# Kernel tuning notes

Hardware: AMD Instinct MI355X
Metric: run time of the kernel (lower is better)

The kernel has to match this reference:

```python
import jax, jax.numpy as jnp
import numpy as np

B, H, E, V, T, EOS = 128, 512, 256, 32000, 32, 0

def setup_inputs() -> dict:
    key = jax.random.key(0)
    ks = jax.random.split(key, 10)
    s_emb = 1.0 / np.sqrt(V)
    s_rnn = 1.0 / np.sqrt(H)
    return {
        "z": jax.random.normal(ks[0], (B, H), jnp.float32),
        "W_emb": jax.random.uniform(ks[1], (E, V), jnp.float32, -s_emb, s_emb),
        "b_emb": jax.random.uniform(ks[2], (E,), jnp.float32, -s_emb, s_emb),
        "W_ih": jax.random.uniform(ks[3], (H, E), jnp.float32, -s_rnn, s_rnn),
        "b_ih": jax.random.uniform(ks[4], (H,), jnp.float32, -s_rnn, s_rnn),
        "W_hh": jax.random.uniform(ks[5], (H, H), jnp.float32, -s_rnn, s_rnn),
        "b_hh": jax.random.uniform(ks[6], (H,), jnp.float32, -s_rnn, s_rnn),
        "W_lin": jax.random.uniform(ks[7], (V, H), jnp.float32, -s_rnn, s_rnn),
        "b_lin": jax.random.uniform(ks[8], (V,), jnp.float32, -s_rnn, s_rnn),
        "train": 0,
    }

def _emit(hidden, W_lin, b_lin):
    # [B,H] @ [H,V] -> log_p [B,V]; greedy (argmax) decode path (train=False)
    log_p = jax.nn.log_softmax(hidden @ W_lin.T + b_lin, axis=-1)
    sample = jnp.argmax(log_p, axis=-1)                       # [B] int
    symb = jax.nn.one_hot(sample, V, dtype=log_p.dtype)       # [B,V]
    lp_tok = jnp.take_along_axis(log_p, sample[:, None], axis=1)[:, 0]
    return symb, lp_tok

def reference(z, W_emb, b_emb, W_ih, b_ih, W_hh, b_hh, W_lin, b_lin, train):
    # step 0: hidden = z, no RNN update
    symb, lp_tok = _emit(z, W_lin, b_lin)
    log_p_sent = lp_tok
    mask = 1.0 - symb[:, EOS]

    def step(carry, _):
        hidden, symb, log_p_sent, mask = carry
        emb = symb @ W_emb.T + b_emb                          # one-hot "embedding" linear
        hidden = jnp.tanh(emb @ W_ih.T + b_ih + hidden @ W_hh.T + b_hh)  # Elman RNN cell
        symb, lp_tok = _emit(hidden, W_lin, b_lin)
        log_p_sent = log_p_sent + mask * lp_tok
        mask = mask * (1.0 - symb[:, EOS])
        return (hidden, symb, log_p_sent, mask), symb

    (_, _, log_p_sent, _), rest = jax.lax.scan(step, (z, symb, log_p_sent, mask), None, length=T - 1)
    sentences = jnp.concatenate([symb[None], rest], axis=0)   # [T,B,V]
    return sentences, log_p_sent
```

## Files before the change

### kernel.cpp

```cpp
#include <hip/hip_runtime.h>
#include <math.h>

constexpr int NB = 128;
constexpr int NH = 512;
constexpr int NE = 256;
constexpr int NV = 32000;
constexpr int NT = 32;
constexpr int NVBW = 1000;

typedef _Float16 half8 __attribute__((ext_vector_type(8)));
typedef float    f32x4 __attribute__((ext_vector_type(4)));

#define AGLD(p)    __hip_atomic_load((p), __ATOMIC_RELAXED, __HIP_MEMORY_SCOPE_AGENT)
#define AGST(p, v) __hip_atomic_store((p), (v), __ATOMIC_RELAXED, __HIP_MEMORY_SCOPE_AGENT)

__global__ void init_kernel(unsigned* cnt) { *cnt = 0u; }

__device__ __forceinline__ void gsync(unsigned* cnt, unsigned target) {
    asm volatile("s_waitcnt vmcnt(0) lgkmcnt(0)" ::: "memory");
    __syncthreads();
    if (threadIdx.x == 0) {
        __hip_atomic_fetch_add(cnt, 1u, __ATOMIC_RELAXED, __HIP_MEMORY_SCOPE_AGENT);
        while (AGLD(cnt) < target) __builtin_amdgcn_s_sleep(4);
    }
    __syncthreads();
    asm volatile("" ::: "memory");
}

__global__ __launch_bounds__(512, 2)
void speaker_kernel(const float* __restrict__ z,    const float* __restrict__ Wemb,
                    const float* __restrict__ bemb, const float* __restrict__ Wih,
                    const float* __restrict__ bih,  const float* __restrict__ Whh,
                    const float* __restrict__ bhh,  const float* __restrict__ Wlin,
                    const float* __restrict__ blin, float* __restrict__ out,
                    _Float16* __restrict__ Wh,      unsigned long long* __restrict__ hidh64,
                    float* __restrict__ hid,
                    float* __restrict__ pm1, int* __restrict__ pi1,
                    float* __restrict__ pm2, int* __restrict__ pi2,
                    float* __restrict__ ps,  float* __restrict__ lps,
                    float* __restrict__ maskp, unsigned* __restrict__ cnt)
{
    __shared__ _Float16 smA[128][64];
    __shared__ _Float16 smB[2][128][64];
    __shared__ float red8[8];
    __shared__ int   cand[32];
    __shared__ float cval[32];
    __shared__ int   ncand;
    __shared__ int   besti;
    __shared__ float es[NE];
    __shared__ float hs[NH];
    __shared__ _Float16 hsout[NH];

    const int blk  = blockIdx.x;
    const int tid  = threadIdx.x;
    const int w    = tid >> 6;
    const int lane = tid & 63;
    const int gtid = blk * 512 + tid;
    constexpr int GT = 256 * 512;
    unsigned sno = 0;

    unsigned long long* Wh64 = (unsigned long long*)Wh;

    for (int i = gtid; i < NV * NH / 4; i += GT) {
        float4 a = ((const float4*)Wlin)[i];
        union { _Float16 h[4]; unsigned long long u; } p;
        p.h[0] = (_Float16)a.x; p.h[1] = (_Float16)a.y;
        p.h[2] = (_Float16)a.z; p.h[3] = (_Float16)a.w;
        AGST(Wh64 + i, p.u);
    }
    for (int i = gtid; i < NB * NH / 4; i += GT) {
        float4 a = ((const float4*)z)[i];
        union { _Float16 h[4]; unsigned long long u; } p;
        p.h[0] = (_Float16)a.x; p.h[1] = (_Float16)a.y;
        p.h[2] = (_Float16)a.z; p.h[3] = (_Float16)a.w;
        AGST(hidh64 + i, p.u);
    }
    ++sno; gsync(cnt, sno * 256u);

    for (int t = 0; t < NT; t++) {
        if (blk < 250) {
            const int wm = w >> 2;
            const int wn = w & 3;
            const int v0 = blk * 128;

            const _Float16* gpB[2];
            unsigned ldsoffB[2];
#pragma unroll
            for (int c = 0; c < 2; c++) {
                int slot = w * 128 + c * 64 + lane;
                int r    = slot >> 3;
                int sp   = slot & 7;
                int g    = sp ^ (r & 7);
                gpB[c] = Wh + (size_t)(v0 + r) * NH + g * 8;
                ldsoffB[c] = (unsigned)(w * 128 + c * 64) * 16;
            }
#define STAGE_B(dbuf, k0)                                                      \
    do {                                                                       \
        _Pragma("unroll")                                                      \
        for (int c = 0; c < 2; c++) {                                          \
            __builtin_amdgcn_global_load_lds(                                  \
                (const __attribute__((address_space(1))) unsigned*)(gpB[c] + (k0)), \
                (__attribute__((address_space(3))) unsigned*)((char*)&smB[0][0][0] + (dbuf)*16384 + ldsoffB[c]), \
                16, 0, 0);                                                     \
        }                                                                      \
    } while (0)

            const int ar   = tid >> 2;
            const int asp0 = (tid & 3) * 2;
            const int ag0  = asp0 ^ (ar & 7);
            const int ag1  = (asp0 + 1) ^ (ar & 7);
            const unsigned long long* hbase = hidh64 + ar * 128;

            f32x4 acc[4][2];
#pragma unroll
            for (int mi = 0; mi < 4; mi++)
#pragma unroll
                for (int ni = 0; ni < 2; ni++) acc[mi][ni] = {0.f, 0.f, 0.f, 0.f};

            unsigned long long a0, a1, a2, a3;
            a0 = AGLD(hbase + ag0 * 2);     a1 = AGLD(hbase + ag0 * 2 + 1);
            a2 = AGLD(hbase + ag1 * 2);     a3 = AGLD(hbase + ag1 * 2 + 1);
            STAGE_B(0, 0);

#pragma unroll
            for (int kt = 0; kt < 8; kt++) {
                {
                    unsigned long long* dA = (unsigned long long*)&smA[ar][asp0 * 8];
                    dA[0] = a0; dA[1] = a1; dA[2] = a2; dA[3] = a3;
                }
                if (kt < 7) {
                    const unsigned long long* hb = hbase + (kt + 1) * 16;
                    a0 = AGLD(hb + ag0 * 2); a1 = AGLD(hb + ag0 * 2 + 1);
                    a2 = AGLD(hb + ag1 * 2); a3 = AGLD(hb + ag1 * 2 + 1);
                    STAGE_B((kt + 1) & 1, (kt + 1) * 64);
                }
                __builtin_amdgcn_sched_barrier(0);
                if (kt < 7) asm volatile("s_waitcnt vmcnt(6)" ::: "memory");
                else        asm volatile("s_waitcnt vmcnt(0)" ::: "memory");
                __builtin_amdgcn_sched_barrier(0);
                __syncthreads();

#pragma unroll
                for (int kk = 0; kk < 2; kk++) {
                    const int sbase = kk * 4 + (lane >> 4);
                    half8 af[4], bf[2];
#pragma unroll
                    for (int mi = 0; mi < 4; mi++) {
                        int r = wm * 64 + mi * 16 + (lane & 15);
                        af[mi] = *(const half8*)&smA[r][(sbase ^ (r & 7)) * 8];
                    }
#pragma unroll
                    for (int ni = 0; ni < 2; ni++) {
                        int rb = wn * 32 + ni * 16 + (lane & 15);
                        bf[ni] = *(const half8*)&smB[kt & 1][rb][(sbase ^ (rb & 7)) * 8];
                    }
#pragma unroll
                    for (int mi = 0; mi < 4; mi++)
#pragma unroll
                        for (int ni = 0; ni < 2; ni++)
                            acc[mi][ni] = __builtin_amdgcn_mfma_f32_16x16x32_f16(
                                af[mi], bf[ni], acc[mi][ni], 0, 0, 0);
                }
                __syncthreads();
            }
#undef STAGE_B

            const int colbase = v0 + wn * 32 + (lane & 15);
            const float bias0 = blin[colbase];
            const float bias1 = blin[colbase + 16];
            const int cidx = blk * 4 + wn;

#pragma unroll
            for (int mi = 0; mi < 4; mi++) {
#pragma unroll
                for (int reg = 0; reg < 4; reg++) {
                    const int bRow = wm * 64 + mi * 16 + (lane >> 4) * 4 + reg;
                    const float va = acc[mi][0][reg] + bias0;
                    const float vc = acc[mi][1][reg] + bias1;
                    float v1, v2; int j1, j2;
                    if (va >= vc) { v1 = va; j1 = colbase;      v2 = vc; j2 = colbase + 16; }
                    else          { v1 = vc; j1 = colbase + 16; v2 = va; j2 = colbase; }
#pragma unroll
                    for (int off = 1; off < 16; off <<= 1) {
                        float o1 = __shfl_xor(v1, off), o2 = __shfl_xor(v2, off);
                        int   k1 = __shfl_xor(j1, off), k2 = __shfl_xor(j2, off);
                        float n1, n2; int m1, m2;
                        bool ob = (o1 > v1) || (o1 == v1 && k1 < j1);
                        if (ob) {
                            n1 = o1; m1 = k1;
                            bool t2 = (v1 > o2) || (v1 == o2 && j1 < k2);
                            if (t2) { n2 = v1; m2 = j1; } else { n2 = o2; m2 = k2; }
                        } else {
                            n1 = v1; m1 = j1;
                            bool t2 = (o1 > v2) || (o1 == v2 && k1 < j2);
                            if (t2) { n2 = o1; m2 = k1; } else { n2 = v2; m2 = j2; }
                        }
                        v1 = n1; j1 = m1; v2 = n2; j2 = m2;
                    }
                    float s = __expf(va - v1) + __expf(vc - v1);
#pragma unroll
                    for (int off = 1; off < 16; off <<= 1) s += __shfl_xor(s, off);
                    if ((lane & 15) == 0) {
                        const int idx = bRow * NVBW + cidx;
                        AGST(pm1 + idx, v1);  AGST(pi1 + idx, j1);
                        AGST(pm2 + idx, v2);  AGST(pi2 + idx, j2);
                        AGST(ps + idx, s);
                    }
                }
            }
        }
        ++sno; gsync(cnt, sno * 256u);

        if (blk < NB) {
            constexpr float DELTA = 0.01f;
            constexpr int   MAXC  = 32;
            const int b = blk;
            const float* hid_in = (t == 0) ? z : hid;

            {
                const float4 zz = {0.f, 0.f, 0.f, 0.f};
                float4* orow = (float4*)(out + (size_t)t * NB * NV + (size_t)b * NV);
                for (int i = tid; i < NV / 4; i += 512) orow[i] = zz;
            }
            hs[tid] = hid_in[(size_t)b * NH + tid];
            if (tid == 0) ncand = 0;
            asm volatile("s_waitcnt vmcnt(0)" ::: "memory");
            __syncthreads();

            float m_ = -1e30f;
            for (int c = tid; c < NVBW; c += 512)
                m_ = fmaxf(m_, AGLD(pm1 + b * NVBW + c));
#pragma unroll
            for (int off = 1; off < 64; off <<= 1) m_ = fmaxf(m_, __shfl_xor(m_, off));
            if (lane == 0) red8[w] = m_;
            __syncthreads();
            const float gmax = fmaxf(fmaxf(fmaxf(red8[0], red8[1]), fmaxf(red8[2], red8[3])),
                                     fmaxf(fmaxf(red8[4], red8[5]), fmaxf(red8[6], red8[7])));
            __syncthreads();

            float s = 0.f;
            for (int c = tid; c < NVBW; c += 512) {
                float p1 = AGLD(pm1 + b * NVBW + c);
                s += AGLD(ps + b * NVBW + c) * __expf(p1 - gmax);
                if (p1 >= gmax - DELTA) {
                    int pos = atomicAdd(&ncand, 1);
                    if (pos < MAXC) cand[pos] = AGLD(pi1 + b * NVBW + c);
                }
                float p2 = AGLD(pm2 + b * NVBW + c);
                if (p2 >= gmax - DELTA) {
                    int pos = atomicAdd(&ncand, 1);
                    if (pos < MAXC) cand[pos] = AGLD(pi2 + b * NVBW + c);
                }
            }
#pragma unroll
            for (int off = 1; off < 64; off <<= 1) s += __shfl_xor(s, off);
            if (lane == 0) red8[w] = s;
            __syncthreads();
            const float tot = ((red8[0] + red8[1]) + (red8[2] + red8[3]))
                            + ((red8[4] + red8[5]) + (red8[6] + red8[7]));
            const int nc = min(ncand, MAXC);

            for (int ci = w; ci < nc; ci += 8) {
                int tok = cand[ci];
                float4 h0 = ((const float4*)hs)[lane * 2];
                float4 h1 = ((const float4*)hs)[lane * 2 + 1];
                const float4* wv = (const float4*)(Wlin + (size_t)tok * NH);
                float4 w0 = wv[lane * 2], w1 = wv[lane * 2 + 1];
                float d = h0.x * w0.x + h0.y * w0.y + h0.z * w0.z + h0.w * w0.w
                        + h1.x * w1.x + h1.y * w1.y + h1.z * w1.z + h1.w * w1.w;
#pragma unroll
                for (int off = 1; off < 64; off <<= 1) d += __shfl_xor(d, off);
                if (lane == 0) cval[ci] = d + blin[tok];
            }
            __syncthreads();

            if (tid == 0) {
                float bv = cval[0]; int bi = cand[0];
                for (int ci = 1; ci < nc; ci++)
                    if (cval[ci] > bv || (cval[ci] == bv && cand[ci] < bi)) { bv = cval[ci]; bi = cand[ci]; }
                float lp = (bv - gmax) - logf(tot);
                float lpv, mk;
                if (t == 0) { lpv = lp; mk = (bi == 0) ? 0.f : 1.f; }
                else {
                    lpv = lps[b]; mk = maskp[b];
                    lpv += mk * lp;
                    mk *= (bi == 0) ? 0.f : 1.f;
                }
                lps[b] = lpv; maskp[b] = mk;
                out[(size_t)t * NB * NV + (size_t)b * NV + bi] = 1.0f;
                if (t == NT - 1) out[(size_t)NT * NB * NV + b] = lpv;
                besti = bi;
            }
            __syncthreads();
            const int gi = besti;

            if (t < NT - 1) {
                if (tid < NE) es[tid] = Wemb[(size_t)tid * NV + gi] + bemb[tid];
                __syncthreads();

                const int h = tid;
                float acc = bih[h] + bhh[h];
                const float4* wi = (const float4*)(Wih + (size_t)h * NE);
#pragma unroll 4
                for (int e4 = 0; e4 < NE / 4; e4++) {
                    float4 ww = wi[e4];
                    acc += ww.x * es[e4 * 4] + ww.y * es[e4 * 4 + 1]
                         + ww.z * es[e4 * 4 + 2] + ww.w * es[e4 * 4 + 3];
                }
                const float4* wh = (const float4*)(Whh + (size_t)h * NH);
#pragma unroll 4
                for (int k4 = 0; k4 < NH / 4; k4++) {
                    float4 ww = wh[k4];
                    acc += ww.x * hs[k4 * 4] + ww.y * hs[k4 * 4 + 1]
                         + ww.z * hs[k4 * 4 + 2] + ww.w * hs[k4 * 4 + 3];
                }
                float v = tanhf(acc);
                hid[(size_t)b * NH + h] = v;
                hsout[h] = (_Float16)v;
                __syncthreads();
                if (tid < 256) {
                    union { _Float16 h2[2]; unsigned u; } p;
                    p.h2[0] = hsout[2 * tid]; p.h2[1] = hsout[2 * tid + 1];
                    AGST((unsigned*)hidh64 + b * 256 + tid, p.u);
                }
            }
        }
        ++sno; gsync(cnt, sno * 256u);
    }
}

extern "C" void kernel_launch(void* const* d_in, const int* in_sizes, int n_in,
                              void* d_out, int out_size, void* d_ws, size_t ws_size,
                              hipStream_t stream) {
    const float* z    = (const float*)d_in[0];
    const float* Wemb = (const float*)d_in[1];
    const float* bemb = (const float*)d_in[2];
    const float* Wih  = (const float*)d_in[3];
    const float* bih  = (const float*)d_in[4];
    const float* Whh  = (const float*)d_in[5];
    const float* bhh  = (const float*)d_in[6];
    const float* Wlin = (const float*)d_in[7];
    const float* blin = (const float*)d_in[8];
    float* out = (float*)d_out;

    char* ws = (char*)d_ws;
    _Float16* Wh  = (_Float16*)(ws);
    unsigned long long* hidh64 = (unsigned long long*)(ws + 32768000);
    float*    hid   = (float*)(ws + 32899072);
    float*    pm1   = (float*)(ws + 33161216);
    int*      pi1   = (int*)  (ws + 33673216);
    float*    pm2   = (float*)(ws + 34185216);
    int*      pi2   = (int*)  (ws + 34697216);
    float*    ps    = (float*)(ws + 35209216);
    float*    lps   = (float*)(ws + 35721216);
    float*    maskp = (float*)(ws + 35721728);
    unsigned* cnt   = (unsigned*)(ws + 35722240);

    init_kernel<<<1, 1, 0, stream>>>(cnt);

    void* args[] = {
        (void*)&z, (void*)&Wemb, (void*)&bemb, (void*)&Wih, (void*)&bih,
        (void*)&Whh, (void*)&bhh, (void*)&Wlin, (void*)&blin, (void*)&out,
        (void*)&Wh, (void*)&hidh64, (void*)&hid,
        (void*)&pm1, (void*)&pi1, (void*)&pm2, (void*)&pi2, (void*)&ps,
        (void*)&lps, (void*)&maskp, (void*)&cnt
    };
    hipLaunchCooperativeKernel((void*)speaker_kernel, dim3(256), dim3(512),
                               args, 0, stream);
}
```

Baseline: 3.605 ms.

## Restructure persistent decode: async A staging, per-step buffers, offloaded zero-fill

The GEMM phase now stages both the hidden-state tile and the weight tile into LDS via global_load_lds, instead of loading A through registers with atomic loads. Hidden states and partial max/sum buffers are indexed per timestep so that plain loads can replace atomic loads, and partials are written coalesced through LDS. Zeroing of the one-hot output moves from the serial per-row reduction blocks to the idle blocks, which zero the next step's slice. Launch bounds drop to one block per CU and LDS is a single arena. The cost is a much larger workspace and looser synchronization assumptions around non-atomic reads after the grid barrier.

```diff
diff --git a/kernel.cpp b/kernel.cpp
--- a/kernel.cpp
+++ b/kernel.cpp
@@ -10,6 +10,7 @@
 
 typedef _Float16 half8 __attribute__((ext_vector_type(8)));
 typedef float    f32x4 __attribute__((ext_vector_type(4)));
+typedef unsigned long long u64;
 
 #define AGLD(p)    __hip_atomic_load((p), __ATOMIC_RELAXED, __HIP_MEMORY_SCOPE_AGENT)
 #define AGST(p, v) __hip_atomic_store((p), (v), __ATOMIC_RELAXED, __HIP_MEMORY_SCOPE_AGENT)
@@ -27,29 +28,34 @@
     asm volatile("" ::: "memory");
 }
 
-__global__ __launch_bounds__(512, 2)
+__global__ __launch_bounds__(512, 1)
 void speaker_kernel(const float* __restrict__ z,    const float* __restrict__ Wemb,
                     const float* __restrict__ bemb, const float* __restrict__ Wih,
                     const float* __restrict__ bih,  const float* __restrict__ Whh,
                     const float* __restrict__ bhh,  const float* __restrict__ Wlin,
                     const float* __restrict__ blin, float* __restrict__ out,
-                    _Float16* __restrict__ Wh,      unsigned long long* __restrict__ hidh64,
+                    _Float16* __restrict__ Wh,      _Float16* __restrict__ hidh,
                     float* __restrict__ hid,
                     float* __restrict__ pm1, int* __restrict__ pi1,
                     float* __restrict__ pm2, int* __restrict__ pi2,
                     float* __restrict__ ps,  float* __restrict__ lps,
                     float* __restrict__ maskp, unsigned* __restrict__ cnt)
 {
-    __shared__ _Float16 smA[128][64];
-    __shared__ _Float16 smB[2][128][64];
-    __shared__ float red8[8];
-    __shared__ int   cand[32];
-    __shared__ float cval[32];
-    __shared__ int   ncand;
-    __shared__ int   besti;
-    __shared__ float es[NE];
-    __shared__ float hs[NH];
-    __shared__ _Float16 hsout[NH];
+    __shared__ __align__(16) char arena[75776];
+    _Float16* smp  = (_Float16*)arena;
+    float*    SV1  = (float*)(arena + 65536);
+    float*    SV2  = (float*)(arena + 67584);
+    float*    SSe  = (float*)(arena + 69632);
+    int*      SJ1  = (int*)  (arena + 71680);
+    int*      SJ2  = (int*)  (arena + 73728);
+    float*    hsf  = (float*)arena;
+    float*    esf  = (float*)(arena + 2048);
+    _Float16* hof  = (_Float16*)(arena + 3072);
+    float*    red8 = (float*)(arena + 4096);
+    int*      candp= (int*)  (arena + 4128);
+    float*    cvalp= (float*)(arena + 4256);
+    int*      ncp  = (int*)  (arena + 4384);
+    int*      bip  = (int*)  (arena + 4388);
 
     const int blk  = blockIdx.x;
     const int tid  = threadIdx.x;
@@ -59,87 +65,77 @@
     constexpr int GT = 256 * 512;
     unsigned sno = 0;
 
-    unsigned long long* Wh64 = (unsigned long long*)Wh;
+    u64* Wh64   = (u64*)Wh;
+    u64* hidh64 = (u64*)hidh;
 
     for (int i = gtid; i < NV * NH / 4; i += GT) {
         float4 a = ((const float4*)Wlin)[i];
-        union { _Float16 h[4]; unsigned long long u; } p;
+        union { _Float16 h[4]; u64 u; } p;
         p.h[0] = (_Float16)a.x; p.h[1] = (_Float16)a.y;
         p.h[2] = (_Float16)a.z; p.h[3] = (_Float16)a.w;
         AGST(Wh64 + i, p.u);
     }
     for (int i = gtid; i < NB * NH / 4; i += GT) {
         float4 a = ((const float4*)z)[i];
-        union { _Float16 h[4]; unsigned long long u; } p;
+        union { _Float16 h[4]; u64 u; } p;
         p.h[0] = (_Float16)a.x; p.h[1] = (_Float16)a.y;
         p.h[2] = (_Float16)a.z; p.h[3] = (_Float16)a.w;
         AGST(hidh64 + i, p.u);
     }
+    for (int i = gtid; i < NB * NV / 2; i += GT) AGST((u64*)out + i, 0ull);
+    if (gtid < 64) AGST((u64*)(out + (size_t)NT * NB * NV) + gtid, 0ull);
     ++sno; gsync(cnt, sno * 256u);
+
+    const int eb = (blk & 7) * 16 + (blk >> 3);
 
     for (int t = 0; t < NT; t++) {
         if (blk < 250) {
             const int wm = w >> 2;
             const int wn = w & 3;
             const int v0 = blk * 128;
-
-            const _Float16* gpB[2];
-            unsigned ldsoffB[2];
-#pragma unroll
-            for (int c = 0; c < 2; c++) {
-                int slot = w * 128 + c * 64 + lane;
-                int r    = slot >> 3;
+            const _Float16* Abase = hidh + (size_t)t * NB * NH;
+
+            const _Float16* gp[4];
+            unsigned ldsoff[4];
+#pragma unroll
+            for (int c = 0; c < 4; c++) {
+                int slot = w * 256 + c * 64 + lane;
+                int mat  = slot >> 10;
+                int r    = (slot >> 3) & 127;
                 int sp   = slot & 7;
-                int g    = sp ^ (r & 7);
-                gpB[c] = Wh + (size_t)(v0 + r) * NH + g * 8;
-                ldsoffB[c] = (unsigned)(w * 128 + c * 64) * 16;
-            }
-#define STAGE_B(dbuf, k0)                                                      \
+                int s    = sp ^ (r & 7);
+                const _Float16* base = mat ? (Wh + (size_t)(v0 + r) * NH)
+                                           : (Abase + (size_t)r * NH);
+                gp[c] = base + s * 8;
+                ldsoff[c] = (unsigned)(w * 256 + c * 64) * 16;
+            }
+
+#define STAGE(db, k0)                                                          \
     do {                                                                       \
         _Pragma("unroll")                                                      \
-        for (int c = 0; c < 2; c++) {                                          \
+        for (int c = 0; c < 4; c++) {                                          \
             __builtin_amdgcn_global_load_lds(                                  \
-                (const __attribute__((address_space(1))) unsigned*)(gpB[c] + (k0)), \
-                (__attribute__((address_space(3))) unsigned*)((char*)&smB[0][0][0] + (dbuf)*16384 + ldsoffB[c]), \
+                (const __attribute__((address_space(1))) unsigned*)(gp[c] + (k0)), \
+                (__attribute__((address_space(3))) unsigned*)(arena + (db) * 32768 + ldsoff[c]), \
                 16, 0, 0);                                                     \
         }                                                                      \
     } while (0)
 
-            const int ar   = tid >> 2;
-            const int asp0 = (tid & 3) * 2;
-            const int ag0  = asp0 ^ (ar & 7);
-            const int ag1  = (asp0 + 1) ^ (ar & 7);
-            const unsigned long long* hbase = hidh64 + ar * 128;
-
             f32x4 acc[4][2];
 #pragma unroll
             for (int mi = 0; mi < 4; mi++)
 #pragma unroll
                 for (int ni = 0; ni < 2; ni++) acc[mi][ni] = {0.f, 0.f, 0.f, 0.f};
 
-            unsigned long long a0, a1, a2, a3;
-            a0 = AGLD(hbase + ag0 * 2);     a1 = AGLD(hbase + ag0 * 2 + 1);
-            a2 = AGLD(hbase + ag1 * 2);     a3 = AGLD(hbase + ag1 * 2 + 1);
-            STAGE_B(0, 0);
-
-#pragma unroll
+            STAGE(0, 0);
+            asm volatile("s_waitcnt vmcnt(0)" ::: "memory");
+            __builtin_amdgcn_sched_barrier(0);
+            __builtin_amdgcn_s_barrier();
+
+            int db = 0;
+#pragma unroll 1
             for (int kt = 0; kt < 8; kt++) {
-                {
-                    unsigned long long* dA = (unsigned long long*)&smA[ar][asp0 * 8];
-                    dA[0] = a0; dA[1] = a1; dA[2] = a2; dA[3] = a3;
-                }
-                if (kt < 7) {
-                    const unsigned long long* hb = hbase + (kt + 1) * 16;
-                    a0 = AGLD(hb + ag0 * 2); a1 = AGLD(hb + ag0 * 2 + 1);
-                    a2 = AGLD(hb + ag1 * 2); a3 = AGLD(hb + ag1 * 2 + 1);
-                    STAGE_B((kt + 1) & 1, (kt + 1) * 64);
-                }
-                __builtin_amdgcn_sched_barrier(0);
-                if (kt < 7) asm volatile("s_waitcnt vmcnt(6)" ::: "memory");
-                else        asm volatile("s_waitcnt vmcnt(0)" ::: "memory");
-                __builtin_amdgcn_sched_barrier(0);
-                __syncthreads();
-
+                if (kt < 7) STAGE(db ^ 1, (kt + 1) * 64);
 #pragma unroll
                 for (int kk = 0; kk < 2; kk++) {
                     const int sbase = kk * 4 + (lane >> 4);
@@ -147,12 +143,12 @@
 #pragma unroll
                     for (int mi = 0; mi < 4; mi++) {
                         int r = wm * 64 + mi * 16 + (lane & 15);
-                        af[mi] = *(const half8*)&smA[r][(sbase ^ (r & 7)) * 8];
+                        af[mi] = *(const half8*)&smp[((db * 2 + 0) * 128 + r) * 64 + ((sbase ^ (r & 7)) * 8)];
                     }
 #pragma unroll
                     for (int ni = 0; ni < 2; ni++) {
                         int rb = wn * 32 + ni * 16 + (lane & 15);
-                        bf[ni] = *(const half8*)&smB[kt & 1][rb][(sbase ^ (rb & 7)) * 8];
+                        bf[ni] = *(const half8*)&smp[((db * 2 + 1) * 128 + rb) * 64 + ((sbase ^ (rb & 7)) * 8)];
                     }
 #pragma unroll
                     for (int mi = 0; mi < 4; mi++)
@@ -161,9 +157,12 @@
                             acc[mi][ni] = __builtin_amdgcn_mfma_f32_16x16x32_f16(
                                 af[mi], bf[ni], acc[mi][ni], 0, 0, 0);
                 }
-                __syncthreads();
-            }
-#undef STAGE_B
+                asm volatile("s_waitcnt vmcnt(0)" ::: "memory");
+                __builtin_amdgcn_sched_barrier(0);
+                __builtin_amdgcn_s_barrier();
+                db ^= 1;
+            }
+#undef STAGE
 
             const int colbase = v0 + wn * 32 + (lane & 15);
             const float bias0 = blin[colbase];
@@ -174,7 +173,6 @@
             for (int mi = 0; mi < 4; mi++) {
 #pragma unroll
                 for (int reg = 0; reg < 4; reg++) {
-                    const int bRow = wm * 64 + mi * 16 + (lane >> 4) * 4 + reg;
                     const float va = acc[mi][0][reg] + bias0;
                     const float vc = acc[mi][1][reg] + bias1;
                     float v1, v2; int j1, j2;
@@ -201,12 +199,20 @@
 #pragma unroll
                     for (int off = 1; off < 16; off <<= 1) s += __shfl_xor(s, off);
                     if ((lane & 15) == 0) {
-                        const int idx = bRow * NVBW + cidx;
-                        AGST(pm1 + idx, v1);  AGST(pi1 + idx, j1);
-                        AGST(pm2 + idx, v2);  AGST(pi2 + idx, j2);
-                        AGST(ps + idx, s);
+                        const int idx = mi * 16 + (lane >> 4) * 4 + reg;
+                        SV1[w * 64 + idx] = v1;  SJ1[w * 64 + idx] = j1;
+                        SV2[w * 64 + idx] = v2;  SJ2[w * 64 + idx] = j2;
+                        SSe[w * 64 + idx] = s;
                     }
                 }
+            }
+            {
+                const size_t gOff = ((size_t)t * NVBW + cidx) * NB + wm * 64 + lane;
+                AGST(pm1 + gOff, SV1[w * 64 + lane]);
+                AGST(pi1 + gOff, SJ1[w * 64 + lane]);
+                AGST(pm2 + gOff, SV2[w * 64 + lane]);
+                AGST(pi2 + gOff, SJ2[w * 64 + lane]);
+                AGST(ps  + gOff, SSe[w * 64 + lane]);
             }
         }
         ++sno; gsync(cnt, sno * 256u);
@@ -214,22 +220,20 @@
         if (blk < NB) {
             constexpr float DELTA = 0.01f;
             constexpr int   MAXC  = 32;
-            const int b = blk;
+            const int b = eb;
             const float* hid_in = (t == 0) ? z : hid;
-
-            {
-                const float4 zz = {0.f, 0.f, 0.f, 0.f};
-                float4* orow = (float4*)(out + (size_t)t * NB * NV + (size_t)b * NV);
-                for (int i = tid; i < NV / 4; i += 512) orow[i] = zz;
-            }
-            hs[tid] = hid_in[(size_t)b * NH + tid];
-            if (tid == 0) ncand = 0;
-            asm volatile("s_waitcnt vmcnt(0)" ::: "memory");
+            const float* pm1t = pm1 + (size_t)t * NVBW * NB;
+            const float* pm2t = pm2 + (size_t)t * NVBW * NB;
+            const float* pst  = ps  + (size_t)t * NVBW * NB;
+            const int*   pi1t = pi1 + (size_t)t * NVBW * NB;
+            const int*   pi2t = pi2 + (size_t)t * NVBW * NB;
+
+            hsf[tid] = hid_in[(size_t)b * NH + tid];
+            if (tid == 0) *ncp = 0;
             __syncthreads();
 
             float m_ = -1e30f;
-            for (int c = tid; c < NVBW; c += 512)
-                m_ = fmaxf(m_, AGLD(pm1 + b * NVBW + c));
+            for (int c = tid; c < NVBW; c += 512) m_ = fmaxf(m_, pm1t[c * NB + b]);
 #pragma unroll
             for (int off = 1; off < 64; off <<= 1) m_ = fmaxf(m_, __shfl_xor(m_, off));
             if (lane == 0) red8[w] = m_;
@@ -240,16 +244,16 @@
 
             float s = 0.f;
             for (int c = tid; c < NVBW; c += 512) {
-                float p1 = AGLD(pm1 + b * NVBW + c);
-                s += AGLD(ps + b * NVBW + c) * __expf(p1 - gmax);
+                float p1 = pm1t[c * NB + b];
+                s += pst[c * NB + b] * __expf(p1 - gmax);
                 if (p1 >= gmax - DELTA) {
-                    int pos = atomicAdd(&ncand, 1);
-                    if (pos < MAXC) cand[pos] = AGLD(pi1 + b * NVBW + c);
-                }
-                float p2 = AGLD(pm2 + b * NVBW + c);
+                    int pos = atomicAdd(ncp, 1);
+                    if (pos < MAXC) candp[pos] = pi1t[c * NB + b];
+                }
+                float p2 = pm2t[c * NB + b];
                 if (p2 >= gmax - DELTA) {
-                    int pos = atomicAdd(&ncand, 1);
-                    if (pos < MAXC) cand[pos] = AGLD(pi2 + b * NVBW + c);
+                    int pos = atomicAdd(ncp, 1);
+                    if (pos < MAXC) candp[pos] = pi2t[c * NB + b];
                 }
             }
 #pragma unroll
@@ -258,26 +262,26 @@
             __syncthreads();
             const float tot = ((red8[0] + red8[1]) + (red8[2] + red8[3]))
                             + ((red8[4] + red8[5]) + (red8[6] + red8[7]));
-            const int nc = min(ncand, MAXC);
+            const int nc = min(*ncp, MAXC);
 
             for (int ci = w; ci < nc; ci += 8) {
-                int tok = cand[ci];
-                float4 h0 = ((const float4*)hs)[lane * 2];
-                float4 h1 = ((const float4*)hs)[lane * 2 + 1];
+                int tok = candp[ci];
+                float4 h0 = ((const float4*)hsf)[lane * 2];
+                float4 h1 = ((const float4*)hsf)[lane * 2 + 1];
                 const float4* wv = (const float4*)(Wlin + (size_t)tok * NH);
                 float4 w0 = wv[lane * 2], w1 = wv[lane * 2 + 1];
                 float d = h0.x * w0.x + h0.y * w0.y + h0.z * w0.z + h0.w * w0.w
                         + h1.x * w1.x + h1.y * w1.y + h1.z * w1.z + h1.w * w1.w;
 #pragma unroll
                 for (int off = 1; off < 64; off <<= 1) d += __shfl_xor(d, off);
-                if (lane == 0) cval[ci] = d + blin[tok];
+                if (lane == 0) cvalp[ci] = d + blin[tok];
             }
             __syncthreads();
 
             if (tid == 0) {
-                float bv = cval[0]; int bi = cand[0];
+                float bv = cvalp[0]; int bi = candp[0];
                 for (int ci = 1; ci < nc; ci++)
-                    if (cval[ci] > bv || (cval[ci] == bv && cand[ci] < bi)) { bv = cval[ci]; bi = cand[ci]; }
+                    if (cvalp[ci] > bv || (cvalp[ci] == bv && candp[ci] < bi)) { bv = cvalp[ci]; bi = candp[ci]; }
                 float lp = (bv - gmax) - logf(tot);
                 float lpv, mk;
                 if (t == 0) { lpv = lp; mk = (bi == 0) ? 0.f : 1.f; }
@@ -287,15 +291,15 @@
                     mk *= (bi == 0) ? 0.f : 1.f;
                 }
                 lps[b] = lpv; maskp[b] = mk;
-                out[(size_t)t * NB * NV + (size_t)b * NV + bi] = 1.0f;
-                if (t == NT - 1) out[(size_t)NT * NB * NV + b] = lpv;
-                besti = bi;
-            }
-            __syncthreads();
-            const int gi = besti;
+                AGST(out + (size_t)t * NB * NV + (size_t)b * NV + bi, 1.0f);
+                if (t == NT - 1) AGST(out + (size_t)NT * NB * NV + b, lpv);
+                *bip = bi;
+            }
+            __syncthreads();
+            const int gi = *bip;
 
             if (t < NT - 1) {
-                if (tid < NE) es[tid] = Wemb[(size_t)tid * NV + gi] + bemb[tid];
+                if (tid < NE) esf[tid] = Wemb[(size_t)tid * NV + gi] + bemb[tid];
                 __syncthreads();
 
                 const int h = tid;
@@ -304,26 +308,30 @@
 #pragma unroll 4
                 for (int e4 = 0; e4 < NE / 4; e4++) {
                     float4 ww = wi[e4];
-                    acc += ww.x * es[e4 * 4] + ww.y * es[e4 * 4 + 1]
-                         + ww.z * es[e4 * 4 + 2] + ww.w * es[e4 * 4 + 3];
+                    acc += ww.x * esf[e4 * 4] + ww.y * esf[e4 * 4 + 1]
+                         + ww.z * esf[e4 * 4 + 2] + ww.w * esf[e4 * 4 + 3];
                 }
                 const float4* wh = (const float4*)(Whh + (size_t)h * NH);
 #pragma unroll 4
                 for (int k4 = 0; k4 < NH / 4; k4++) {
                     float4 ww = wh[k4];
-                    acc += ww.x * hs[k4 * 4] + ww.y * hs[k4 * 4 + 1]
-                         + ww.z * hs[k4 * 4 + 2] + ww.w * hs[k4 * 4 + 3];
+                    acc += ww.x * hsf[k4 * 4] + ww.y * hsf[k4 * 4 + 1]
+                         + ww.z * hsf[k4 * 4 + 2] + ww.w * hsf[k4 * 4 + 3];
                 }
                 float v = tanhf(acc);
                 hid[(size_t)b * NH + h] = v;
-                hsout[h] = (_Float16)v;
+                hof[h] = (_Float16)v;
                 __syncthreads();
                 if (tid < 256) {
                     union { _Float16 h2[2]; unsigned u; } p;
-                    p.h2[0] = hsout[2 * tid]; p.h2[1] = hsout[2 * tid + 1];
-                    AGST((unsigned*)hidh64 + b * 256 + tid, p.u);
-                }
-            }
+                    p.h2[0] = hof[2 * tid]; p.h2[1] = hof[2 * tid + 1];
+                    AGST((unsigned*)(hidh + (size_t)(t + 1) * NB * NH + (size_t)b * NH) + tid, p.u);
+                }
+            }
+        } else if (t < NT - 1) {
+            u64* dst = (u64*)(out + (size_t)(t + 1) * NB * NV);
+            for (int i = (blk - 128) * 512 + tid; i < NB * NV / 2; i += 128 * 512)
+                AGST(dst + i, 0ull);
         }
         ++sno; gsync(cnt, sno * 256u);
     }
@@ -344,24 +352,24 @@
     float* out = (float*)d_out;
 
     char* ws = (char*)d_ws;
-    _Float16* Wh  = (_Float16*)(ws);
-    unsigned long long* hidh64 = (unsigned long long*)(ws + 32768000);
-    float*    hid   = (float*)(ws + 32899072);
-    float*    pm1   = (float*)(ws + 33161216);
-    int*      pi1   = (int*)  (ws + 33673216);
-    float*    pm2   = (float*)(ws + 34185216);
-    int*      pi2   = (int*)  (ws + 34697216);
-    float*    ps    = (float*)(ws + 35209216);
-    float*    lps   = (float*)(ws + 35721216);
-    float*    maskp = (float*)(ws + 35721728);
-    unsigned* cnt   = (unsigned*)(ws + 35722240);
+    _Float16* Wh    = (_Float16*)(ws);
+    _Float16* hidh  = (_Float16*)(ws + 32768000);
+    float*    hid   = (float*)   (ws + 36962304);
+    float*    pm1   = (float*)   (ws + 37224448);
+    int*      pi1   = (int*)     (ws + 53608448);
+    float*    pm2   = (float*)   (ws + 69992448);
+    int*      pi2   = (int*)     (ws + 86376448);
+    float*    ps    = (float*)   (ws + 102760448);
+    float*    lps   = (float*)   (ws + 119144448);
+    float*    maskp = (float*)   (ws + 119144960);
+    unsigned* cnt   = (unsigned*)(ws + 119145472);
 
     init_kernel<<<1, 1, 0, stream>>>(cnt);
 
     void* args[] = {
         (void*)&z, (void*)&Wemb, (void*)&bemb, (void*)&Wih, (void*)&bih,
         (void*)&Whh, (void*)&bhh, (void*)&Wlin, (void*)&blin, (void*)&out,
-        (void*)&Wh, (void*)&hidh64, (void*)&hid,
+        (void*)&Wh, (void*)&hidh, (void*)&hid,
         (void*)&pm1, (void*)&pi1, (void*)&pm2, (void*)&pi2, (void*)&ps,
         (void*)&lps, (void*)&maskp, (void*)&cnt
     };
```

New measurement: 3.179 ms. 11.8% less time.
